# Kernel tuning notes

Hardware: AMD Instinct MI355X
Metric: run time of the kernel (lower is better)

The kernel has to match this reference:

```python
import jax, jax.numpy as jnp
import numpy as np

B, T, NH, HS = 2, 2048, 16, 64
C = NH * HS
V_SHIFT = 1          # value shift; queries start at position V_SHIFT
EXP_SCALE = 10.0     # exp_param_scale
KB_UP = 5.0          # kernel_beta_upbound


def setup_inputs() -> dict:
    key = jax.random.key(0)
    ks = jax.random.split(key, 8)
    s = 0.02
    return {
        "x": jax.random.normal(ks[0], (B, T, C), jnp.float32),
        # leaky-average key path: linear proj + per-head decay coefficient
        "W_la": jax.random.normal(ks[1], (C, C), jnp.float32) * s,
        "la_coef": jax.random.uniform(ks[2], (NH,), jnp.float32, 0.1, 0.9),
        "kernel_beta": jnp.ones((NH,), jnp.float32) / EXP_SCALE,
        "value_beta": jnp.ones((NH,), jnp.float32) * (-0.5) / EXP_SCALE,
        # value featurizer (lowrlinearconv): linear + per-head mixing coef
        "W_v": jax.random.normal(ks[3], (C, C), jnp.float32) * s,
        "v_coef": jax.random.uniform(ks[4], (NH,), jnp.float32, 0.0, 1.0),
        "W_proj": jax.random.normal(ks[5], (C, C), jnp.float32) * s,
    }


def reference(x, W_la, la_coef, kernel_beta, value_beta, W_v, v_coef, W_proj):
    B_, T_, C_ = x.shape
    # ---- keys: leaky average (per-head EMA recurrence) of linear projection ----
    xl = (x @ W_la).reshape(B_, T_, NH, HS)          # (B,T,nh,hs)
    alpha = la_coef.reshape(NH, 1)                   # per-head decay

    def step(carry, xt):  # carry,xt: (B,nh,hs)
        new = alpha * carry + (1.0 - alpha) * xt
        return new, new

    _, kt = jax.lax.scan(step, jnp.zeros((B_, NH, HS), x.dtype),
                         jnp.swapaxes(xl, 0, 1))    # (T,B,nh,hs)
    k = jnp.transpose(kt, (1, 2, 0, 3))              # (B,nh,T,hs)
    k = k / jnp.linalg.norm(k, axis=-1, keepdims=True)
    kb = jnp.exp(jnp.minimum(kernel_beta * EXP_SCALE, KB_UP)).reshape(1, NH, 1, 1)
    k = k * kb

    # ---- values: lowrlinearconv featurizer (shift=1, kernel=2) + L2 norm ----
    xv = (x @ W_v).reshape(B_, T_, NH, HS).transpose(0, 2, 1, 3)   # (B,nh,T,hs)
    xv_sh = jnp.concatenate([xv[:, :, 1:], jnp.zeros_like(xv[:, :, :1])], axis=2)
    c = v_coef.reshape(1, NH, 1, 1)
    v = xv_sh * (1.0 - c) + xv * c
    v = v / jnp.linalg.norm(v, axis=-1, keepdims=True)
    v = v * jnp.exp(value_beta * EXP_SCALE).reshape(1, NH, 1, 1)

    # ---- shifted-causal masked SDPA (scale=1); queries are positions >= V_SHIFT ----
    q = k[:, :, V_SHIFT:]                            # (B,nh,T-1,hs)
    scores = jnp.einsum('bhqd,bhkd->bhqk', q, k)
    qpos = jnp.arange(V_SHIFT, T_)[:, None]
    kpos = jnp.arange(T_)[None, :]
    mask = kpos < qpos                               # key j visible iff j < query position
    scores = jnp.where(mask, scores, -jnp.inf)
    att = jax.nn.softmax(scores, axis=-1)
    y_att = jnp.einsum('bhqk,bhkd->bhqd', att, v)
    y = jnp.concatenate([jnp.zeros((B_, NH, V_SHIFT, HS), x.dtype), y_att], axis=2)
    y = jnp.transpose(y, (0, 2, 1, 3)).reshape(B_, T_, C_)
    return y @ W_proj                                # dropouts are eval-mode identity
```

## Files before the change

kernel.cpp:

```cpp
#include <hip/hip_runtime.h>
#include <hip/hip_bf16.h>

#define B_  2
#define T_  2048
#define NH_ 16
#define HS_ 64
#define C_  1024
#define SCL_ 128
#define SCN_ (T_ / SCL_)
#define NT_  (T_ / 64)
#define TEL_ 4096

typedef __attribute__((ext_vector_type(8))) short bf16x8;
typedef __attribute__((ext_vector_type(4))) float f32x4;

__device__ inline int pack_bf16(float a, float b) {
  union { __hip_bfloat16 h; unsigned short u; } ua, ub;
  ua.h = __float2bfloat16(a);
  ub.h = __float2bfloat16(b);
  return (int)(((unsigned)ub.u << 16) | (unsigned)ua.u);
}

__device__ inline void gl_lds16(const __hip_bfloat16* g, __hip_bfloat16* l) {
  __builtin_amdgcn_global_load_lds(
      (const __attribute__((address_space(1))) unsigned int*)g,
      (__attribute__((address_space(3))) unsigned int*)l, 16, 0, 0);
}

__global__ __launch_bounds__(256) void prep1_kernel(const float* __restrict__ x,
                                                    const float* __restrict__ W_la,
                                                    const float* __restrict__ W_v,
                                                    const float* __restrict__ W_proj,
                                                    __hip_bfloat16* __restrict__ x16,
                                                    __hip_bfloat16* __restrict__ Wcat,
                                                    __hip_bfloat16* __restrict__ WprojT) {
  __shared__ __hip_bfloat16 tile[64][66];
  const int bid = (int)blockIdx.x;
  if (bid < 2048) {
    const int i = (bid * 256 + (int)threadIdx.x) * 8;
    const float4 a = *reinterpret_cast<const float4*>(x + i);
    const float4 b = *reinterpret_cast<const float4*>(x + i + 4);
    union { int s[4]; int4 v; } u;
    u.s[0] = pack_bf16(a.x, a.y);
    u.s[1] = pack_bf16(a.z, a.w);
    u.s[2] = pack_bf16(b.x, b.y);
    u.s[3] = pack_bf16(b.z, b.w);
    *reinterpret_cast<int4*>(x16 + i) = u.v;
    return;
  }
  const int id = bid - 2048;
  const int z = id >> 8;
  const int rem = id & 255;
  const int bx = rem & 15, by = rem >> 4;
  const float* W = (z == 0) ? W_la : (z == 1) ? W_v : W_proj;
  __hip_bfloat16* WT = (z == 2) ? WprojT : Wcat + (size_t)z * C_ * C_;
  const int w = threadIdx.x >> 6, l = threadIdx.x & 63;
  const int n0 = bx * 64, k0 = by * 64;
#pragma unroll
  for (int r = 0; r < 16; ++r) {
    const int k = k0 + w * 16 + r;
    tile[w * 16 + r][l] = __float2bfloat16(W[(size_t)k * C_ + n0 + l]);
  }
  __syncthreads();
#pragma unroll
  for (int r = 0; r < 16; ++r) {
    const int nn = w * 16 + r;
    WT[(size_t)(n0 + nn) * C_ + k0 + l] = tile[l][nn];
  }
}

__global__ __launch_bounds__(256) void gemm_in_kernel(const __hip_bfloat16* __restrict__ A,
                                                      const __hip_bfloat16* __restrict__ BT,
                                                      float* __restrict__ C0,
                                                      float* __restrict__ C1) {
  __shared__ __hip_bfloat16 As[2 * 128 * 32];
  __shared__ __hip_bfloat16 Bs[2 * 128 * 32];
  const int tid = threadIdx.x;
  const int m0 = blockIdx.y * 128, n0 = blockIdx.x * 128;
  const int w = tid >> 6, l = tid & 63;
  const int n = l & 15, kg = l >> 4;
  const int m0w = (w & 1) * 64, n0w = (w >> 1) * 64;

  const int r0 = tid >> 2, o0 = (tid & 3) * 8;
  const __hip_bfloat16* ag0 = A + (size_t)(m0 + r0) * C_ + o0;
  const __hip_bfloat16* ag1 = A + (size_t)(m0 + 64 + r0) * C_ + o0;
  const __hip_bfloat16* bg0 = BT + (size_t)(n0 + r0) * C_ + o0;
  const __hip_bfloat16* bg1 = BT + (size_t)(n0 + 64 + r0) * C_ + o0;

  f32x4 acc[4][4];
#pragma unroll
  for (int i = 0; i < 4; ++i)
#pragma unroll
    for (int j = 0; j < 4; ++j) acc[i][j] = f32x4{0.f, 0.f, 0.f, 0.f};

  auto stage = [&](int kk, int buf) {
    __hip_bfloat16* a = As + buf * 4096;
    __hip_bfloat16* b = Bs + buf * 4096;
    gl_lds16(ag0 + kk, a + tid * 8);
    gl_lds16(ag1 + kk, a + 2048 + tid * 8);
    gl_lds16(bg0 + kk, b + tid * 8);
    gl_lds16(bg1 + kk, b + 2048 + tid * 8);
  };

  stage(0, 0);
  int cur = 0;
  for (int k0 = 0; k0 < C_; k0 += 32) {
    asm volatile("" ::: "memory");
    __builtin_amdgcn_s_barrier();
    asm volatile("" ::: "memory");
    if (k0 + 32 < C_) {
      stage(k0 + 32, cur ^ 1);
      asm volatile("s_waitcnt vmcnt(4)" ::: "memory");
    } else {
      asm volatile("s_waitcnt vmcnt(0)" ::: "memory");
    }
    __builtin_amdgcn_s_barrier();
    asm volatile("" ::: "memory");

    const __hip_bfloat16* Ab = As + cur * 4096;
    const __hip_bfloat16* Bb = Bs + cur * 4096;
    bf16x8 af[4], bf[4];
#pragma unroll
    for (int ms = 0; ms < 4; ++ms)
      af[ms] = *reinterpret_cast<const bf16x8*>(Ab + (m0w + ms * 16 + n) * 32 + kg * 8);
#pragma unroll
    for (int ns = 0; ns < 4; ++ns)
      bf[ns] = *reinterpret_cast<const bf16x8*>(Bb + (n0w + ns * 16 + n) * 32 + kg * 8);
#pragma unroll
    for (int ms = 0; ms < 4; ++ms)
#pragma unroll
      for (int ns = 0; ns < 4; ++ns)
        acc[ms][ns] = __builtin_amdgcn_mfma_f32_16x16x32_bf16(af[ms], bf[ns], acc[ms][ns], 0, 0, 0);
    cur ^= 1;
  }

  float* Cb = (n0 < C_) ? C0 : C1;
  const int nc = (n0 < C_) ? n0 : n0 - C_;
#pragma unroll
  for (int ms = 0; ms < 4; ++ms) {
#pragma unroll
    for (int r = 0; r < 4; ++r) {
      const int row = m0 + m0w + ms * 16 + kg * 4 + r;
      float* cp = Cb + (size_t)row * C_ + nc + n0w + n;
#pragma unroll
      for (int ns = 0; ns < 4; ++ns) cp[ns * 16] = acc[ms][ns][r];
    }
  }
}

__global__ __launch_bounds__(256) void gemm_proj_kernel(const __hip_bfloat16* __restrict__ A,
                                                        const __hip_bfloat16* __restrict__ BT,
                                                        float* __restrict__ Cout) {
  __shared__ __hip_bfloat16 As[2 * 64 * 32];
  __shared__ __hip_bfloat16 Bs[2 * 128 * 32];
  const int tid = threadIdx.x;
  const int m0 = blockIdx.y * 64, n0 = blockIdx.x * 128;
  const int w = tid >> 6, l = tid & 63;
  const int n = l & 15, kg = l >> 4;

  const int r0 = tid >> 2, o0 = (tid & 3) * 8;
  const __hip_bfloat16* ag = A + (size_t)(m0 + r0) * C_ + o0;
  const __hip_bfloat16* bg0 = BT + (size_t)(n0 + r0) * C_ + o0;
  const __hip_bfloat16* bg1 = BT + (size_t)(n0 + 64 + r0) * C_ + o0;

  f32x4 acc[4][2];
#pragma unroll
  for (int i = 0; i < 4; ++i)
#pragma unroll
    for (int j = 0; j < 2; ++j) acc[i][j] = f32x4{0.f, 0.f, 0.f, 0.f};

  auto stage = [&](int kk, int buf) {
    __hip_bfloat16* a = As + buf * 2048;
    __hip_bfloat16* b = Bs + buf * 4096;
    gl_lds16(ag + kk, a + tid * 8);
    gl_lds16(bg0 + kk, b + tid * 8);
    gl_lds16(bg1 + kk, b + 2048 + tid * 8);
  };

  stage(0, 0);
  int cur = 0;
  for (int k0 = 0; k0 < C_; k0 += 32) {
    asm volatile("" ::: "memory");
    __builtin_amdgcn_s_barrier();
    asm volatile("" ::: "memory");
    if (k0 + 32 < C_) {
      stage(k0 + 32, cur ^ 1);
      asm volatile("s_waitcnt vmcnt(3)" ::: "memory");
    } else {
      asm volatile("s_waitcnt vmcnt(0)" ::: "memory");
    }
    __builtin_amdgcn_s_barrier();
    asm volatile("" ::: "memory");

    const __hip_bfloat16* Ab = As + cur * 2048;
    const __hip_bfloat16* Bb = Bs + cur * 4096;
    bf16x8 af[4], bf[2];
#pragma unroll
    for (int ms = 0; ms < 4; ++ms)
      af[ms] = *reinterpret_cast<const bf16x8*>(Ab + (ms * 16 + n) * 32 + kg * 8);
#pragma unroll
    for (int ns = 0; ns < 2; ++ns)
      bf[ns] = *reinterpret_cast<const bf16x8*>(Bb + (w * 32 + ns * 16 + n) * 32 + kg * 8);
#pragma unroll
    for (int ms = 0; ms < 4; ++ms)
#pragma unroll
      for (int ns = 0; ns < 2; ++ns)
        acc[ms][ns] = __builtin_amdgcn_mfma_f32_16x16x32_bf16(af[ms], bf[ns], acc[ms][ns], 0, 0, 0);
    cur ^= 1;
  }

#pragma unroll
  for (int ms = 0; ms < 4; ++ms) {
#pragma unroll
    for (int r = 0; r < 4; ++r) {
      const int row = m0 + ms * 16 + kg * 4 + r;
      float* cp = Cout + (size_t)row * C_ + n0 + w * 32 + n;
#pragma unroll
      for (int ns = 0; ns < 2; ++ns) cp[ns * 16] = acc[ms][ns][r];
    }
  }
}

__global__ __launch_bounds__(256) void prep2_kernel(const float* __restrict__ xv,
                                                    const float* __restrict__ xl,
                                                    __hip_bfloat16* __restrict__ vt,
                                                    __hip_bfloat16* __restrict__ kb16,
                                                    const float* __restrict__ value_beta,
                                                    const float* __restrict__ v_coef,
                                                    const float* __restrict__ la_coef,
                                                    const float* __restrict__ kernel_beta) {
  __shared__ float4 smem4[2048];
  const int bid = (int)blockIdx.x;
  if (bid < 1024) {
    __hip_bfloat16 (*tile)[66] = reinterpret_cast<__hip_bfloat16(*)[66]>(smem4);
    const int tc = bid % NT_;
    const int bh = bid / NT_;
    const int h = bh % NH_, b = bh / NH_;
    const int t0 = tc * 64;
    const int w = threadIdx.x >> 6, l = threadIdx.x & 63;

    const float c = v_coef[h];
    const float vb = expf(value_beta[h] * 10.0f);

    for (int r = 0; r < 16; ++r) {
      const int tl = w * 16 + r;
      const int t = t0 + tl;
      const float* base = xv + ((size_t)b * T_ + t) * C_ + h * HS_ + l;
      const float cu = base[0];
      const float nxt = (t + 1 < T_) ? base[C_] : 0.0f;
      float val = nxt * (1.0f - c) + cu * c;
      float ssum = val * val;
#pragma unroll
      for (int m = 32; m; m >>= 1) ssum += __shfl_xor(ssum, m);
      tile[tl][l] = __float2bfloat16(val * (vb / sqrtf(ssum)));
    }
    __syncthreads();
    __hip_bfloat16* vtb = vt + (size_t)(bh * NT_ + tc) * TEL_;
    const int kk = l >> 3, j = l & 7;
    for (int rr = 0; rr < 16; ++rr) {
      const int hs = w * 16 + rr;
      vtb[(kk * 64 + hs) * 8 + j] = tile[l][hs];
    }
    return;
  }
  {
    float* buf = reinterpret_cast<float*>(smem4);
    const int idx = bid - 1024;
    const int c = idx % SCN_;
    const int bh = idx / SCN_;
    const int b = bh / NH_, h = bh % NH_;
    const int tid = threadIdx.x;

    const float alpha = la_coef[h];
    const float onema = 1.0f - alpha;
    const float kbs = expf(fminf(kernel_beta[h] * 10.0f, 5.0f));
    const float4* src4 = reinterpret_cast<const float4*>(xl + (size_t)b * T_ * C_ + h * HS_);
    float4* buf4 = reinterpret_cast<float4*>(buf);

    float A = 0.0f;
    if (c > 0) {
      const int t0p = (c - 1) * SCL_;
#pragma unroll
      for (int i = 0; i < 8; ++i) {
        const int ix = tid + i * 256;
        const int tt = ix >> 4, d4 = ix & 15;
        buf4[tt * 16 + d4] = src4[(size_t)(t0p + tt) * (C_ / 4) + d4];
      }
      __syncthreads();
      if (tid < 64) {
        const int d = tid;
#pragma unroll 8
        for (int tt = 0; tt < SCL_; ++tt)
          A = alpha * A + onema * buf[tt * HS_ + d];
      }
      __syncthreads();
    }
    const int t0 = c * SCL_;
#pragma unroll
    for (int i = 0; i < 8; ++i) {
      const int ix = tid + i * 256;
      const int tt = ix >> 4, d4 = ix & 15;
      buf4[tt * 16 + d4] = src4[(size_t)(t0 + tt) * (C_ / 4) + d4];
    }
    __syncthreads();
    if (tid < 64) {
      const int d = tid;
#pragma unroll 8
      for (int tt = 0; tt < SCL_; ++tt) {
        A = alpha * A + onema * buf[tt * HS_ + d];
        buf[tt * HS_ + d] = A;
      }
    }
    __syncthreads();
    const int w = tid >> 6, l = tid & 63;
    __hip_bfloat16* kt = kb16 + (size_t)bh * NT_ * TEL_;
    const int g = l >> 3, j = l & 7;
    for (int rr = 0; rr < 32; ++rr) {
      const int tl = w * 32 + rr;
      const int t = t0 + tl;
      const float val = buf[tl * HS_ + l];
      float ss = val * val;
#pragma unroll
      for (int m = 32; m; m >>= 1) ss += __shfl_xor(ss, m);
      const int tile = t >> 6, key = t & 63;
      kt[(size_t)tile * TEL_ + (g * 64 + key) * 8 + j] = __float2bfloat16(val * (kbs / sqrtf(ss)));
    }
  }
}

__global__ __launch_bounds__(256, 4) void attn_mfma_kernel(
    const __hip_bfloat16* __restrict__ kb,
    const __hip_bfloat16* __restrict__ vt,
    __hip_bfloat16* __restrict__ y) {
  __shared__ __hip_bfloat16 Ks[2][2 * TEL_];
  __shared__ __hip_bfloat16 Ps[4][16 * 64];

  const int id = (int)blockIdx.x;
  const int xcd = id & 7;
  const int s = id >> 3;
  const int bh = xcd + 8 * (s & 3);
  const int v = s >> 2;
  const int qt = (v < 16) ? (31 - v) : (v - 16);
  const int b = bh / NH_, h = bh % NH_;
  const int q0 = qt * 64;
  const int w = threadIdx.x >> 6;
  const int l = threadIdx.x & 63;
  const int n = l & 15;
  const int kg = l >> 4;
  const int qq = w * 16 + n;
  const int query = q0 + qq;
  const int lo = l * 8;
  const int tb = bh * NT_;
  const int so = w * 1024 + lo;

  bf16x8 qf0, qf1;
  {
    const __hip_bfloat16* qtile = kb + (size_t)(tb + qt) * TEL_;
    qf0 = *reinterpret_cast<const bf16x8*>(qtile + (kg * 64 + qq) * 8);
    qf1 = *reinterpret_cast<const bf16x8*>(qtile + ((kg + 4) * 64 + qq) * 8);
  }
  const __hip_bfloat16* vbase = vt + (size_t)tb * TEL_ + (kg * 64 + n) * 8;

  f32x4 accO[4];
#pragma unroll
  for (int i = 0; i < 4; ++i) accO[i] = f32x4{0.f, 0.f, 0.f, 0.f};
  float l_acc = 0.0f;

  __hip_bfloat16* Pw = Ps[w];
  int* Pwi = reinterpret_cast<int*>(Pw);

  auto stage2 = [&](int j0, int buf) {
    const size_t tg = (size_t)(tb + j0) * TEL_;
    __hip_bfloat16* Kb = &Ks[buf][0];
    gl_lds16(kb + tg + so, Kb + so);
    gl_lds16(kb + tg + so + 512, Kb + so + 512);
    gl_lds16(kb + tg + TEL_ + so, Kb + TEL_ + so);
    gl_lds16(kb + tg + TEL_ + so + 512, Kb + TEL_ + so + 512);
  };
  auto stage1 = [&](int j0, int buf) {
    const size_t tg = (size_t)(tb + j0) * TEL_;
    __hip_bfloat16* Kb = &Ks[buf][0];
    gl_lds16(kb + tg + so, Kb + so);
    gl_lds16(kb + tg + so + 512, Kb + so + 512);
  };
  auto loadV = [&](int jt, bf16x8 (&vf)[2][4]) {
    const __hip_bfloat16* vp = vbase + (size_t)jt * TEL_;
#pragma unroll
    for (int ks = 0; ks < 2; ++ks)
#pragma unroll
      for (int mo = 0; mo < 4; ++mo)
        vf[ks][mo] = *reinterpret_cast<const bf16x8*>(vp + ks * 2048 + mo * 128);
  };
  auto computeS = [&](const __hip_bfloat16* Kc, f32x4 (&accS)[4]) {
    __builtin_amdgcn_s_setprio(1);
#pragma unroll
    for (int ms = 0; ms < 4; ++ms) {
      bf16x8 a0 = *reinterpret_cast<const bf16x8*>(Kc + (kg * 64 + ms * 16 + n) * 8);
      bf16x8 a1 = *reinterpret_cast<const bf16x8*>(Kc + ((kg + 4) * 64 + ms * 16 + n) * 8);
      f32x4 z{0.f, 0.f, 0.f, 0.f};
      z = __builtin_amdgcn_mfma_f32_16x16x32_bf16(a0, qf0, z, 0, 0, 0);
      accS[ms] = __builtin_amdgcn_mfma_f32_16x16x32_bf16(a1, qf1, z, 0, 0, 0);
    }
    __builtin_amdgcn_s_setprio(0);
  };
  auto softmaxStore = [&](const f32x4 (&accS)[4], bool diag) {
    if (!diag) {
#pragma unroll
      for (int ms = 0; ms < 4; ++ms) {
        const float p0 = __expf(accS[ms][0]), p1 = __expf(accS[ms][1]);
        const float p2 = __expf(accS[ms][2]), p3 = __expf(accS[ms][3]);
        l_acc += p0 + p1 + p2 + p3;
        const int po = n * 32 + (((ms * 4 + kg) ^ n) << 1);
        int2 pw;
        pw.x = pack_bf16(p0, p1);
        pw.y = pack_bf16(p2, p3);
        *reinterpret_cast<int2*>(&Pwi[po]) = pw;
      }
    } else {
#pragma unroll
      for (int ms = 0; ms < 4; ++ms) {
        const int kbase = ms * 16 + kg * 4;
        float p[4];
#pragma unroll
        for (int r = 0; r < 4; ++r) {
          const float e = __expf(accS[ms][r]);
          p[r] = (kbase + r < qq) ? e : 0.0f;
          l_acc += p[r];
        }
        const int po = n * 32 + (((ms * 4 + kg) ^ n) << 1);
        int2 pw;
        pw.x = pack_bf16(p[0], p[1]);
        pw.y = pack_bf16(p[2], p[3]);
        *reinterpret_cast<int2*>(&Pwi[po]) = pw;
      }
    }
  };
  auto pv = [&](const bf16x8 (&vf)[2][4]) {
    __builtin_amdgcn_s_setprio(1);
#pragma unroll
    for (int ks = 0; ks < 2; ++ks) {
      union { ushort4 u[2]; bf16x8 vv; } pr;
      const int ga = (ks * 8 + kg * 2) ^ n;
      const __hip_bfloat16* pp = Pw + n * 64;
      pr.u[0] = *reinterpret_cast<const ushort4*>(pp + ga * 4);
      pr.u[1] = *reinterpret_cast<const ushort4*>(pp + (ga ^ 1) * 4);
#pragma unroll
      for (int mo = 0; mo < 4; ++mo)
        accO[mo] = __builtin_amdgcn_mfma_f32_16x16x32_bf16(vf[ks][mo], pr.vv, accO[mo], 0, 0, 0);
    }
    __builtin_amdgcn_s_setprio(0);
  };

  if (qt >= 1) stage2(0, 0); else stage1(0, 0);

  int cur = 0;
  int jp = 0;
  for (; jp + 1 <= qt; jp += 2) {
    asm volatile("" ::: "memory");
    __builtin_amdgcn_s_barrier();
    asm volatile("" ::: "memory");

    bf16x8 vfA[2][4];
    loadV(jp, vfA);
    asm volatile("" ::: "memory");

    const int nx = jp + 2;
    if (nx + 1 <= qt) {
      stage2(nx, cur ^ 1);
      asm volatile("s_waitcnt vmcnt(12)" ::: "memory");
    } else if (nx <= qt) {
      stage1(nx, cur ^ 1);
      asm volatile("s_waitcnt vmcnt(10)" ::: "memory");
    } else {
      asm volatile("s_waitcnt vmcnt(8)" ::: "memory");
    }
    __builtin_amdgcn_s_barrier();
    asm volatile("" ::: "memory");

    f32x4 accS[4];
    computeS(&Ks[cur][0], accS);
    softmaxStore(accS, false);
    pv(vfA);

    asm volatile("" ::: "memory");

    bf16x8 vfB[2][4];
    loadV(jp + 1, vfB);
    computeS(&Ks[cur][TEL_], accS);
    softmaxStore(accS, jp + 1 == qt);
    pv(vfB);

    cur ^= 1;
  }
  if (jp <= qt) {
    asm volatile("" ::: "memory");
    __builtin_amdgcn_s_barrier();
    asm volatile("" ::: "memory");
    bf16x8 vfA[2][4];
    loadV(jp, vfA);
    asm volatile("s_waitcnt vmcnt(8)" ::: "memory");
    __builtin_amdgcn_s_barrier();
    asm volatile("" ::: "memory");
    f32x4 accS[4];
    computeS(&Ks[cur][0], accS);
    softmaxStore(accS, true);
    pv(vfA);
  }

  l_acc += __shfl_xor(l_acc, 16);
  l_acc += __shfl_xor(l_acc, 32);
  const float inv = (query == 0) ? 0.0f : 1.0f / l_acc;
  __hip_bfloat16* yb = y + ((size_t)b * T_ + query) * C_ + h * HS_;
#pragma unroll
  for (int mo = 0; mo < 4; ++mo) {
    int2 pkd;
    pkd.x = pack_bf16(accO[mo][0] * inv, accO[mo][1] * inv);
    pkd.y = pack_bf16(accO[mo][2] * inv, accO[mo][3] * inv);
    *reinterpret_cast<int2*>(yb + mo * 16 + kg * 4) = pkd;
  }
}

extern "C" void kernel_launch(void* const* d_in, const int* in_sizes, int n_in,
                              void* d_out, int out_size, void* d_ws, size_t ws_size,
                              hipStream_t stream) {
  const float* x           = (const float*)d_in[0];
  const float* W_la        = (const float*)d_in[1];
  const float* la_coef     = (const float*)d_in[2];
  const float* kernel_beta = (const float*)d_in[3];
  const float* value_beta  = (const float*)d_in[4];
  const float* W_v         = (const float*)d_in[5];
  const float* v_coef      = (const float*)d_in[6];
  const float* W_proj      = (const float*)d_in[7];
  float* out = (float*)d_out;

  char* wsb = (char*)d_ws;
  const size_t MB = 1024u * 1024u;
  __hip_bfloat16* x16    = (__hip_bfloat16*)(wsb);
  __hip_bfloat16* Wcat   = (__hip_bfloat16*)(wsb + 8 * MB);
  __hip_bfloat16* WprojT = (__hip_bfloat16*)(wsb + 12 * MB);
  float* xl              = (float*)(wsb + 16 * MB);
  float* xv              = (float*)(wsb + 32 * MB);
  __hip_bfloat16* kb16   = (__hip_bfloat16*)(wsb + 48 * MB);
  __hip_bfloat16* vt16   = (__hip_bfloat16*)(wsb + 56 * MB);
  __hip_bfloat16* y16    = (__hip_bfloat16*)(wsb + 64 * MB);
  (void)ws_size; (void)in_sizes; (void)n_in; (void)out_size;

  const int M = B_ * T_;

  prep1_kernel<<<dim3(2048 + 768), dim3(256), 0, stream>>>(x, W_la, W_v, W_proj, x16, Wcat, WprojT);
  gemm_in_kernel<<<dim3(2 * C_ / 128, M / 128), dim3(256), 0, stream>>>(x16, Wcat, xl, xv);
  prep2_kernel<<<dim3(1024 + 512), dim3(256), 0, stream>>>(xv, xl, vt16, kb16,
                                                           value_beta, v_coef, la_coef, kernel_beta);
  attn_mfma_kernel<<<dim3(8 * 128), dim3(256), 0, stream>>>(kb16, vt16, y16);
  gemm_proj_kernel<<<dim3(C_ / 128, M / 64), dim3(256), 0, stream>>>(y16, WprojT, out);
}
```

Before: 192.1 us.

## Parallelize leaky-average scan across all four waves with segment carries

The EMA recurrence in the prep kernel ran serially on a single wave (64 threads) over 128 timesteps, twice (previous chunk for the carry, then the current chunk). Each of the four waves now scans its own 32-step segment, and the segment carries are combined with alpha^32 powers through shared memory. The scan is then fused into the normalize-and-store loop, so no scanned values are written back to LDS. This cuts the serial dependency chain by 4x at the cost of extra barriers and a pow call, and the reassociated recurrence may change floating-point rounding slightly.

```diff
diff --git a/kernel.cpp b/kernel.cpp
--- a/kernel.cpp
+++ b/kernel.cpp
@@ -230,6 +230,8 @@
                                                     const float* __restrict__ la_coef,
                                                     const float* __restrict__ kernel_beta) {
   __shared__ float4 smem4[2048];
+  __shared__ float carrW[4][64];
+  __shared__ float carrS[4][64];
   const int bid = (int)blockIdx.x;
   if (bid < 1024) {
     __hip_bfloat16 (*tile)[66] = reinterpret_cast<__hip_bfloat16(*)[66]>(smem4);
@@ -270,60 +272,61 @@
     const int bh = idx / SCN_;
     const int b = bh / NH_, h = bh % NH_;
     const int tid = threadIdx.x;
+    const int w = tid >> 6, l = tid & 63;
 
     const float alpha = la_coef[h];
     const float onema = 1.0f - alpha;
+    const float a32 = __powf(alpha, 32.0f);
     const float kbs = expf(fminf(kernel_beta[h] * 10.0f, 5.0f));
     const float4* src4 = reinterpret_cast<const float4*>(xl + (size_t)b * T_ * C_ + h * HS_);
     float4* buf4 = reinterpret_cast<float4*>(buf);
 
-    float A = 0.0f;
-    if (c > 0) {
-      const int t0p = (c - 1) * SCL_;
+    auto stageChunk = [&](int t0s) {
 #pragma unroll
       for (int i = 0; i < 8; ++i) {
         const int ix = tid + i * 256;
         const int tt = ix >> 4, d4 = ix & 15;
-        buf4[tt * 16 + d4] = src4[(size_t)(t0p + tt) * (C_ / 4) + d4];
+        buf4[tt * 16 + d4] = src4[(size_t)(t0s + tt) * (C_ / 4) + d4];
       }
+    };
+    auto localCarry = [&]() -> float {
+      float A = 0.0f;
+      const float* bp = buf + (w * 32) * HS_ + l;
+#pragma unroll 8
+      for (int tt = 0; tt < 32; ++tt) A = alpha * A + onema * bp[tt * HS_];
+      return A;
+    };
+
+    float W = 0.0f;
+    if (c > 0) {
+      stageChunk((c - 1) * SCL_);
       __syncthreads();
-      if (tid < 64) {
-        const int d = tid;
-#pragma unroll 8
-        for (int tt = 0; tt < SCL_; ++tt)
-          A = alpha * A + onema * buf[tt * HS_ + d];
-      }
+      carrW[w][l] = localCarry();
       __syncthreads();
+      W = ((carrW[0][l] * a32 + carrW[1][l]) * a32 + carrW[2][l]) * a32 + carrW[3][l];
     }
     const int t0 = c * SCL_;
-#pragma unroll
-    for (int i = 0; i < 8; ++i) {
-      const int ix = tid + i * 256;
-      const int tt = ix >> 4, d4 = ix & 15;
-      buf4[tt * 16 + d4] = src4[(size_t)(t0 + tt) * (C_ / 4) + d4];
-    }
     __syncthreads();
-    if (tid < 64) {
-      const int d = tid;
-#pragma unroll 8
-      for (int tt = 0; tt < SCL_; ++tt) {
-        A = alpha * A + onema * buf[tt * HS_ + d];
-        buf[tt * HS_ + d] = A;
-      }
-    }
+    stageChunk(t0);
     __syncthreads();
-    const int w = tid >> 6, l = tid & 63;
+    carrS[w][l] = localCarry();
+    __syncthreads();
+    float P = W;
+#pragma unroll
+    for (int j2 = 0; j2 < 3; ++j2)
+      if (j2 < w) P = carrS[j2][l] + a32 * P;
     __hip_bfloat16* kt = kb16 + (size_t)bh * NT_ * TEL_;
     const int g = l >> 3, j = l & 7;
+    const float* bp = buf + (w * 32) * HS_ + l;
+    float A = P;
     for (int rr = 0; rr < 32; ++rr) {
-      const int tl = w * 32 + rr;
-      const int t = t0 + tl;
-      const float val = buf[tl * HS_ + l];
-      float ss = val * val;
+      A = alpha * A + onema * bp[rr * HS_];
+      float ss = A * A;
 #pragma unroll
       for (int m = 32; m; m >>= 1) ss += __shfl_xor(ss, m);
+      const int t = t0 + w * 32 + rr;
       const int tile = t >> 6, key = t & 63;
-      kt[(size_t)tile * TEL_ + (g * 64 + key) * 8 + j] = __float2bfloat16(val * (kbs / sqrtf(ss)));
+      kt[(size_t)tile * TEL_ + (g * 64 + key) * 8 + j] = __float2bfloat16(A * (kbs / sqrtf(ss)));
     }
   }
 }
```

Measured after the change: 192.6 us. Within noise of the previous version (+0.3%).
